# Optimization experiments

Hardware: AMD Instinct MI355X
Metric: run time of the kernel (lower is better)

The kernel has to match this reference:

```python
import jax, jax.numpy as jnp
import numpy as np

B, C_IN, HW = 4096, 3, 32
NUM_MODULES, NUM_AGENTS, OUT_DIM = 16, 10, 10
FEAT = 128
HID = 48
BN_EPS = 1e-5


def _conv_block(x, w, b):
    # x: [B,C,H,W], w: [O,I,3,3] -> conv(pad=1) + ReLU + maxpool2
    y = jax.lax.conv_general_dilated(
        x, w, window_strides=(1, 1), padding=((1, 1), (1, 1)),
        dimension_numbers=("NCHW", "OIHW", "NCHW"))
    y = jax.nn.relu(y + b[None, :, None, None])
    return jax.lax.reduce_window(y, -jnp.inf, jax.lax.max,
                                 (1, 1, 2, 2), (1, 1, 2, 2), "VALID")


def setup_inputs() -> dict:
    key = jax.random.key(0)
    ks = jax.random.split(key, 24)

    def lin(k, shape, fan_in):
        return (jax.random.normal(k, shape, dtype=jnp.float32) / np.sqrt(fan_in)).astype(jnp.float32)

    inp = {
        "x": jax.random.normal(ks[0], (B, C_IN, HW, HW), dtype=jnp.float32),
        "tasks": jax.random.randint(ks[1], (B,), 0, NUM_AGENTS, dtype=jnp.int32),
        # conv backbone
        "cw1": lin(ks[2], (32, C_IN, 3, 3), C_IN * 9), "cb1": jnp.zeros((32,), jnp.float32),
        "cw2": lin(ks[3], (32, 32, 3, 3), 32 * 9),     "cb2": jnp.zeros((32,), jnp.float32),
        "cw3": lin(ks[4], (32, 32, 3, 3), 32 * 9),     "cb3": jnp.zeros((32,), jnp.float32),
        "cw4": lin(ks[5], (32, 32, 3, 3), 32 * 9),     "cb4": jnp.zeros((32,), jnp.float32),
        "bn_g": jnp.ones((32,), jnp.float32), "bn_b": jnp.zeros((32,), jnp.float32),
        # routing policies (approx linear policies)
        "wpt": lin(ks[6], (FEAT, NUM_AGENTS), FEAT),                  # per-task assignment (1 agent)
        "wd1": lin(ks[7], (NUM_AGENTS, FEAT, NUM_MODULES), FEAT),    # per-agent decision 1
        "wd2": lin(ks[8], (NUM_AGENTS, HID, NUM_MODULES), HID),      # per-agent decision 2
        "wd3": lin(ks[9], (NUM_AGENTS, HID, NUM_MODULES), HID),      # per-agent decision 3
        # expert banks (stacked Linear layers, stored [in,out])
        "s1_w": lin(ks[10], (NUM_MODULES, FEAT, HID), FEAT), "s1_b": jnp.zeros((NUM_MODULES, HID), jnp.float32),
        "s2_w": lin(ks[11], (NUM_MODULES, HID, HID), HID),   "s2_b": jnp.zeros((NUM_MODULES, HID), jnp.float32),
        "s3_w": lin(ks[12], (NUM_MODULES, HID, OUT_DIM), HID), "s3_b": jnp.zeros((NUM_MODULES, OUT_DIM), jnp.float32),
    }
    return inp


def _decide(feat, wd, agents):
    # gather per-sample agent policy, pick argmax action
    logits = jnp.einsum("bf,bfm->bm", feat, wd[agents])  # [B, num_modules]
    return jnp.argmax(logits, axis=-1)


def _select(feat, w_bank, b_bank, actions, relu=True):
    # per-sample expert gather -> small GEMM -> scatter back (vectorized)
    y = jnp.einsum("bf,bfo->bo", feat, w_bank[actions]) + b_bank[actions]
    return jax.nn.relu(y) if relu else y


def reference(x, tasks, cw1, cb1, cw2, cb2, cw3, cb3, cw4, cb4, bn_g, bn_b,
              wpt, wd1, wd2, wd3, s1_w, s1_b, s2_w, s2_b, s3_w, s3_b):
    y = _conv_block(x, cw1, cb1)
    y = _conv_block(y, cw2, cb2)
    y = _conv_block(y, cw3, cb3)
    y = _conv_block(y, cw4, cb4)
    # BatchNorm2d (training-mode batch stats)
    mu = jnp.mean(y, axis=(0, 2, 3), keepdims=True)
    var = jnp.var(y, axis=(0, 2, 3), keepdims=True)
    y = (y - mu) * jax.lax.rsqrt(var + BN_EPS) * bn_g[None, :, None, None] + bn_b[None, :, None, None]
    y = y.reshape(y.shape[0], -1)  # [B, 128]

    # per-task assignment: single-agent policy picks the agent id per sample
    task_actions = jnp.argmax(y @ wpt, axis=-1)  # [B]

    a1 = _decide(y, wd1, task_actions)
    y = _select(y, s1_w, s1_b, a1, relu=True)
    a2 = _decide(y, wd2, task_actions)
    y = _select(y, s2_w, s2_b, a2, relu=True)
    a3 = _decide(y, wd3, task_actions)
    y = _select(y, s3_w, s3_b, a3, relu=False)
    return y
```

## Files before the change

### kernel.cpp

```cpp
#include <hip/hip_runtime.h>
#include <math.h>


#define IMG_B 4096

typedef _Float16 f16x8 __attribute__((ext_vector_type(8)));
typedef _Float16 f16x4 __attribute__((ext_vector_type(4)));
typedef float    f32x4 __attribute__((ext_vector_type(4)));

union U16x8 { unsigned u[4]; f16x8 v; };

__device__ inline f16x8 f16x8_zero() {
    f16x8 z;
    #pragma unroll
    for (int i = 0; i < 8; ++i) z[i] = (_Float16)0.f;
    return z;
}

__global__ __launch_bounds__(256) void twt_kernel(
    const float* __restrict__ cw1, const float* __restrict__ cw2,
    const float* __restrict__ cw3, const float* __restrict__ cw4,
    _Float16* __restrict__ w1s, _Float16* __restrict__ w2s,
    _Float16* __restrict__ w3s, _Float16* __restrict__ w4s)
{
    const int i = blockIdx.x * 256 + threadIdx.x;
    if (i < 2048) {
        const int p = i >> 10, rr = i & 1023;
        const int oc = rr >> 5, k = rr & 31;
        _Float16 val = (_Float16)0.f;
        if (k < 27) {
            float w = cw1[oc * 27 + k];
            _Float16 h = (_Float16)w;
            val = p ? (_Float16)(w - (float)h) : h;
        }
        w1s[p * 1024 + oc * 32 + k] = val;
    }
    if (i < 9216) {
        const int k = i % 9, r = i / 9;
        const int ic2 = r & 31, oc2 = r >> 5;
        {
            float w = cw2[(oc2 * 32 + ic2) * 9 + k];
            _Float16 h = (_Float16)w;
            w2s[(k * 2 + 0) * 1024 + oc2 * 32 + ic2] = h;
            w2s[(k * 2 + 1) * 1024 + oc2 * 32 + ic2] = (_Float16)(w - (float)h);
        }
        {
            float w = cw3[(oc2 * 32 + ic2) * 9 + k];
            _Float16 h = (_Float16)w;
            w3s[(k * 2 + 0) * 1024 + oc2 * 32 + ic2] = h;
            w3s[(k * 2 + 1) * 1024 + oc2 * 32 + ic2] = (_Float16)(w - (float)h);
        }
        {
            float w = cw4[(oc2 * 32 + ic2) * 9 + k];
            _Float16 h = (_Float16)w;
            w4s[(k * 2 + 0) * 1024 + oc2 * 32 + ic2] = h;
            w4s[(k * 2 + 1) * 1024 + oc2 * 32 + ic2] = (_Float16)(w - (float)h);
        }
    }
}

__global__ __launch_bounds__(512, 6) void backbone_kernel(
    const float* __restrict__ x,
    const _Float16* __restrict__ w1s, const float* __restrict__ cb1,
    const _Float16* __restrict__ w2s, const float* __restrict__ cb2,
    const _Float16* __restrict__ w3s, const float* __restrict__ cb3,
    const _Float16* __restrict__ w4s, const float* __restrict__ cb4,
    float* __restrict__ t4)
{
    __shared__ __align__(16) unsigned char smem[50736];
    _Float16* b1h = (_Float16*)smem;
    _Float16* b1l = (_Float16*)(smem + 18432);
    unsigned char* region2 = smem + 36864;
    unsigned* sxu = (unsigned*)region2;
    _Float16* b2h = (_Float16*)region2;
    _Float16* b2l = (_Float16*)(region2 + 4096);
    _Float16* b3h = (_Float16*)(region2 + 8192);
    _Float16* b3l = (_Float16*)(region2 + 10496);
    float*    scr = (float*)region2;

    const int t = threadIdx.x;
    const int b = blockIdx.x;
    const int lane = t & 63;
    const int w  = __builtin_amdgcn_readfirstlane(t >> 6);
    const int wr = w >> 1;
    const int mh = w & 1;
    const int xl = lane & 15;
    const int g  = lane >> 4;
    const int aoff = xl * 32 + g * 8;

    for (int i = t; i < 396; i += 512) {
        const int p = i / 132, r = i - p * 132;
        int row, col;
        if (r < 34)       { row = 0;       col = r; }
        else if (r < 68)  { row = 33;      col = r - 34; }
        else if (r < 100) { row = r - 67;  col = 0; }
        else              { row = r - 99;  col = 33; }
        sxu[p * 1156 + row * 34 + col] = 0;
    }
    for (int i = t; i < 1024; i += 512) {
        const int j = i & 15, cs = (i >> 4) & 1, r = (i >> 5) & 15, P = i >> 9;
        ((unsigned*)(smem + P * 18432))[(r * 18 + (cs ? 17 : 0)) * 16 + j] = 0;
    }
    {
        const float* xb = x + (size_t)b * 3072;
        for (int i = t; i < 3072; i += 512) {
            const int ic = i >> 10, r = i & 1023;
            const float v = xb[i];
            const _Float16 h = (_Float16)v;
            const _Float16 l = (_Float16)(v - (float)h);
            const unsigned hu = (unsigned)__builtin_bit_cast(unsigned short, h);
            const unsigned lu = (unsigned)__builtin_bit_cast(unsigned short, l);
            sxu[ic * 1156 + ((r >> 5) + 1) * 34 + (r & 31) + 1] =
                __builtin_amdgcn_perm(lu, hu, 0x05040100u);
        }
    }
    __syncthreads();

    {
        const f16x8 ah0 = *(const f16x8*)(w1s + xl * 32 + g * 8);
        const f16x8 ah1 = *(const f16x8*)(w1s + (16 + xl) * 32 + g * 8);
        const f16x8 al0 = *(const f16x8*)(w1s + 1024 + xl * 32 + g * 8);
        const f16x8 al1 = *(const f16x8*)(w1s + 1024 + (16 + xl) * 32 + g * 8);
        const f32x4 cbias0 = *(const f32x4*)(cb1 + g * 4);
        const f32x4 cbias1 = *(const f32x4*)(cb1 + 16 + g * 4);

        int off_j[8];
        #pragma unroll
        for (int j = 0; j < 8; ++j) {
            int k = g * 8 + j; if (k > 26) k = 26;
            const int ic = k / 9, t9 = k - ic * 9;
            const int dy = t9 / 3, dx = t9 - dy * 3;
            off_j[j] = ic * 1156 + dy * 34 + dx;
        }

        #pragma unroll
        for (int q = 0; q < 2; ++q) {
            const int rp = w * 2 + q;
            const int y0 = 2 * rp;
            #pragma unroll
            for (int xt = 0; xt < 2; ++xt) {
                const int xpix = xt * 16 + xl;
                f32x4 acc[2][2];
                #pragma unroll
                for (int yy = 0; yy < 2; ++yy)
                    #pragma unroll
                    for (int m = 0; m < 2; ++m)
                        #pragma unroll
                        for (int r = 0; r < 4; ++r) acc[yy][m][r] = 0.f;
                #pragma unroll
                for (int yy = 0; yy < 2; ++yy) {
                    const int base = (y0 + yy) * 34 + xpix;
                    unsigned e[8];
                    #pragma unroll
                    for (int j = 0; j < 8; ++j) e[j] = sxu[off_j[j] + base];
                    U16x8 Bh, Bl;
                    #pragma unroll
                    for (int p = 0; p < 4; ++p) {
                        const unsigned e0 = e[2 * p], e1 = e[2 * p + 1];
                        Bh.u[p] = __builtin_amdgcn_perm(e1, e0, 0x05040100u);
                        Bl.u[p] = __builtin_amdgcn_perm(e1, e0, 0x07060302u);
                    }
                    acc[yy][0] = __builtin_amdgcn_mfma_f32_16x16x32_f16(ah0, Bh.v, acc[yy][0], 0, 0, 0);
                    acc[yy][0] = __builtin_amdgcn_mfma_f32_16x16x32_f16(ah0, Bl.v, acc[yy][0], 0, 0, 0);
                    acc[yy][0] = __builtin_amdgcn_mfma_f32_16x16x32_f16(al0, Bh.v, acc[yy][0], 0, 0, 0);
                    acc[yy][1] = __builtin_amdgcn_mfma_f32_16x16x32_f16(ah1, Bh.v, acc[yy][1], 0, 0, 0);
                    acc[yy][1] = __builtin_amdgcn_mfma_f32_16x16x32_f16(ah1, Bl.v, acc[yy][1], 0, 0, 0);
                    acc[yy][1] = __builtin_amdgcn_mfma_f32_16x16x32_f16(al1, Bh.v, acc[yy][1], 0, 0, 0);
                }
                #pragma unroll
                for (int m = 0; m < 2; ++m) {
                    f32x4 vv;
                    #pragma unroll
                    for (int r = 0; r < 4; ++r) {
                        float v = fmaxf(acc[0][m][r], acc[1][m][r]);
                        v = fmaxf(v, __shfl_xor(v, 1));
                        vv[r] = fmaxf(v + (m ? cbias1[r] : cbias0[r]), 0.f);
                    }
                    if ((xl & 1) == 0) {
                        const int c = xt * 8 + (xl >> 1) + 1;
                        const int grp = m * 2 + (g >> 1);
                        const int so = (grp + (c >> 1)) & 3;
                        const int e = (rp * 18 + c) * 32 + so * 8 + (g & 1) * 4;
                        f16x4 h4, l4;
                        #pragma unroll
                        for (int r = 0; r < 4; ++r) {
                            const _Float16 h = (_Float16)vv[r];
                            h4[r] = h;
                            l4[r] = (_Float16)(vv[r] - (float)h);
                        }
                        *(f16x4*)(b1h + e) = h4;
                        *(f16x4*)(b1l + e) = l4;
                    }
                }
            }
        }
    }
    __syncthreads();

    {
        for (int i = t; i < 1152; i += 512) ((unsigned*)(region2 + 8192))[i] = 0;

        f32x4 acc[2][2];
        #pragma unroll
        for (int j = 0; j < 2; ++j)
            #pragma unroll
            for (int m = 0; m < 2; ++m)
                #pragma unroll
                for (int r = 0; r < 4; ++r) acc[j][m][r] = 0.f;

        #pragma unroll
        for (int dy = 0; dy < 3; ++dy) {
            #pragma unroll
            for (int dx = 0; dx < 3; ++dx) {
                const _Float16* wb = w2s + (dy * 3 + dx) * 2048;
                const f16x8 ah0 = *(const f16x8*)(wb + aoff);
                const f16x8 ah1 = *(const f16x8*)(wb + 512 + aoff);
                const f16x8 al0 = *(const f16x8*)(wb + 1024 + aoff);
                const f16x8 al1 = *(const f16x8*)(wb + 1536 + aoff);

                const int cxs = xl + dx;
                const int so = (g + (cxs >> 1)) & 3;
                #pragma unroll
                for (int j = 0; j < 2; ++j) {
                    const int sy = 2 * w + j + dy - 1;
                    if ((unsigned)sy < 16u) {
                        const int e = (sy * 18 + cxs) * 32 + so * 8;
                        const f16x8 bh = *(const f16x8*)(b1h + e);
                        const f16x8 bl = *(const f16x8*)(b1l + e);
                        acc[j][0] = __builtin_amdgcn_mfma_f32_16x16x32_f16(ah0, bh, acc[j][0], 0, 0, 0);
                        acc[j][0] = __builtin_amdgcn_mfma_f32_16x16x32_f16(ah0, bl, acc[j][0], 0, 0, 0);
                        acc[j][0] = __builtin_amdgcn_mfma_f32_16x16x32_f16(al0, bh, acc[j][0], 0, 0, 0);
                        acc[j][1] = __builtin_amdgcn_mfma_f32_16x16x32_f16(ah1, bh, acc[j][1], 0, 0, 0);
                        acc[j][1] = __builtin_amdgcn_mfma_f32_16x16x32_f16(ah1, bl, acc[j][1], 0, 0, 0);
                        acc[j][1] = __builtin_amdgcn_mfma_f32_16x16x32_f16(al1, bh, acc[j][1], 0, 0, 0);
                    }
                }
            }
        }

        const f32x4 bias0 = *(const f32x4*)(cb2 + g * 4);
        const f32x4 bias1 = *(const f32x4*)(cb2 + 16 + g * 4);
        #pragma unroll
        for (int m = 0; m < 2; ++m) {
            f32x4 vv;
            #pragma unroll
            for (int r = 0; r < 4; ++r) {
                float v = fmaxf(acc[0][m][r], acc[1][m][r]);
                v = fmaxf(v, __shfl_xor(v, 1));
                vv[r] = fmaxf(v + (m ? bias1[r] : bias0[r]), 0.f);
            }
            if ((lane & 1) == 0) {
                const int pp = w * 8 + (xl >> 1);
                const int slot = m * 2 + (g >> 1);
                const int so2 = (slot + (pp >> 1)) & 3;
                const int e = pp * 32 + so2 * 8 + (g & 1) * 4;
                f16x4 h4, l4;
                #pragma unroll
                for (int r = 0; r < 4; ++r) {
                    const _Float16 h = (_Float16)vv[r];
                    h4[r] = h;
                    l4[r] = (_Float16)(vv[r] - (float)h);
                }
                *(f16x4*)(b2h + e) = h4;
                *(f16x4*)(b2l + e) = l4;
            }
        }
    }
    __syncthreads();

    {
        const int p = wr * 16 + xl;
        const int py3 = p >> 3, px3 = p & 7;
        f32x4 acc;
        #pragma unroll
        for (int r = 0; r < 4; ++r) acc[r] = 0.f;

        #pragma unroll
        for (int dy = 0; dy < 3; ++dy) {
            #pragma unroll
            for (int dx = 0; dx < 3; ++dx) {
                const _Float16* wb = w3s + (dy * 3 + dx) * 2048 + mh * 512;
                const f16x8 ah = *(const f16x8*)(wb + aoff);
                const f16x8 al = *(const f16x8*)(wb + 1024 + aoff);

                const int syL = py3 + dy - 1, sxL = px3 + dx - 1;
                const bool ok = ((unsigned)syL < 8u) && ((unsigned)sxL < 8u);
                const int cy = syL < 0 ? 0 : (syL > 7 ? 7 : syL);
                const int cx = sxL < 0 ? 0 : (sxL > 7 ? 7 : sxL);
                const int cp = cy * 8 + cx;
                const int so = (g + (cp >> 1)) & 3;
                const int e = cp * 32 + so * 8;
                f16x8 bh = *(const f16x8*)(b2h + e);
                f16x8 bl = *(const f16x8*)(b2l + e);
                if (!ok) { bh = f16x8_zero(); bl = f16x8_zero(); }
                acc = __builtin_amdgcn_mfma_f32_16x16x32_f16(ah, bh, acc, 0, 0, 0);
                acc = __builtin_amdgcn_mfma_f32_16x16x32_f16(ah, bl, acc, 0, 0, 0);
                acc = __builtin_amdgcn_mfma_f32_16x16x32_f16(al, bh, acc, 0, 0, 0);
            }
        }

        const f32x4 bias = *(const f32x4*)(cb3 + mh * 16 + g * 4);
        f32x4 vv;
        #pragma unroll
        for (int r = 0; r < 4; ++r) {
            float v = acc[r];
            v = fmaxf(v, __shfl_xor(v, 1));
            v = fmaxf(v, __shfl_xor(v, 8));
            vv[r] = fmaxf(v + bias[r], 0.f);
        }
        if ((lane & 9) == 0) {
            const int yr = wr;
            const int xr = (xl & 7) >> 1;
            const int pp3 = (yr + 1) * 6 + (xr + 1);
            const int grp = mh * 2 + (g >> 1);
            const int so = (grp + (pp3 >> 1)) & 3;
            const int e = pp3 * 32 + so * 8 + (g & 1) * 4;
            f16x4 h4, l4;
            #pragma unroll
            for (int r = 0; r < 4; ++r) {
                const _Float16 h = (_Float16)vv[r];
                h4[r] = h;
                l4[r] = (_Float16)(vv[r] - (float)h);
            }
            *(f16x4*)(b3h + e) = h4;
            *(f16x4*)(b3l + e) = l4;
        }
    }
    __syncthreads();

    {
        f32x4 a4;
        #pragma unroll
        for (int r = 0; r < 4; ++r) a4[r] = 0.f;

        for (int t9 = wr; t9 < 9; t9 += 4) {
            const _Float16* wb = w4s + t9 * 2048 + mh * 512;
            const f16x8 ah = *(const f16x8*)(wb + aoff);
            const f16x8 al = *(const f16x8*)(wb + 1024 + aoff);
            const int dy = t9 / 3, dx = t9 - dy * 3;
            const int pp3 = ((xl >> 2) + dy) * 6 + (xl & 3) + dx;
            const int so = (g + (pp3 >> 1)) & 3;
            const int e = pp3 * 32 + so * 8;
            const f16x8 bh = *(const f16x8*)(b3h + e);
            const f16x8 bl = *(const f16x8*)(b3l + e);
            a4 = __builtin_amdgcn_mfma_f32_16x16x32_f16(ah, bh, a4, 0, 0, 0);
            a4 = __builtin_amdgcn_mfma_f32_16x16x32_f16(ah, bl, a4, 0, 0, 0);
            a4 = __builtin_amdgcn_mfma_f32_16x16x32_f16(al, bh, a4, 0, 0, 0);
        }
        *(f32x4*)(scr + (w * 64 + lane) * 4) = a4;
        __syncthreads();

        if (w < 2) {
            f32x4 r0;
            #pragma unroll
            for (int r = 0; r < 4; ++r) r0[r] = 0.f;
            #pragma unroll
            for (int k = 0; k < 4; ++k) {
                const f32x4 p0 = *(const f32x4*)(scr + ((k * 2 + w) * 64 + lane) * 4);
                #pragma unroll
                for (int r = 0; r < 4; ++r) r0[r] += p0[r];
            }
            const f32x4 bias = *(const f32x4*)(cb4 + w * 16 + g * 4);
            const int y = xl >> 2, xx = xl & 3;
            f32x4 vv;
            #pragma unroll
            for (int r = 0; r < 4; ++r) {
                float v = r0[r];
                v = fmaxf(v, __shfl_xor(v, 1));
                v = fmaxf(v, __shfl_xor(v, 4));
                vv[r] = fmaxf(v + bias[r], 0.f);
            }
            if ((xl & 5) == 0) {
                const int oc0 = w * 16 + g * 4;
                #pragma unroll
                for (int r = 0; r < 4; ++r)
                    t4[(size_t)b * 128 + (oc0 + r) * 4 + (y >> 1) * 2 + (xx >> 1)] = vv[r];
            }
        }
    }
}

__global__ __launch_bounds__(256) void bnstatsA_kernel(
    const float* __restrict__ t4, double* __restrict__ part)
{
    __shared__ double ssum[256];
    __shared__ double ssq[256];
    const int c = blockIdx.x >> 3, s = blockIdx.x & 7, t = threadIdx.x;
    const float* base = t4 + (size_t)s * 512 * 128 + c * 4;
    double sm = 0.0, q = 0.0;
    for (int j = t; j < 2048; j += 256) {
        const float v = base[(size_t)(j >> 2) * 128 + (j & 3)];
        sm += (double)v;
        q += (double)v * (double)v;
    }
    ssum[t] = sm; ssq[t] = q;
    __syncthreads();
    for (int w = 128; w > 0; w >>= 1) {
        if (t < w) { ssum[t] += ssum[t + w]; ssq[t] += ssq[t + w]; }
        __syncthreads();
    }
    if (t == 0) {
        part[(c * 8 + s) * 2]     = ssum[0];
        part[(c * 8 + s) * 2 + 1] = ssq[0];
    }
}

__global__ __launch_bounds__(256) void bnstatsB_kernel(
    const double* __restrict__ part, float* __restrict__ mus, float* __restrict__ rss)
{
    const int t = threadIdx.x;
    double sm = part[t * 2], q = part[t * 2 + 1];
    #pragma unroll
    for (int d = 1; d < 8; d <<= 1) {
        sm += __shfl_xor(sm, d);
        q += __shfl_xor(q, d);
    }
    if ((t & 7) == 0) {
        const double mu = sm / 16384.0;
        const double var = q / 16384.0 - mu * mu;
        mus[t >> 3] = (float)mu;
        rss[t >> 3] = (float)(1.0 / sqrt(var + 1e-5));
    }
}

__device__ __forceinline__ int wave_argmax16(double v, int idx) {
    #pragma unroll
    for (int d = 8; d >= 1; d >>= 1) {
        const double ov = __shfl_xor(v, d);
        const int oi = __shfl_xor(idx, d);
        if (ov > v || (ov == v && oi < idx)) { v = ov; idx = oi; }
    }
    return __shfl(idx, 0);
}

__global__ __launch_bounds__(256) void routing_kernel(
    const float* __restrict__ t4, const float* __restrict__ mus,
    const float* __restrict__ rss,
    const float* __restrict__ bng, const float* __restrict__ bnb,
    const float* __restrict__ wpt, const float* __restrict__ wd1,
    const float* __restrict__ wd2, const float* __restrict__ wd3,
    const float* __restrict__ s1w, const float* __restrict__ s1b,
    const float* __restrict__ s2w, const float* __restrict__ s2b,
    const float* __restrict__ s3w, const float* __restrict__ s3b,
    float* __restrict__ out)
{
    __shared__ float fs[4][128];
    __shared__ float h1s[4][48];
    __shared__ float h2s[4][48];
    const int t = threadIdx.x & 63;
    const int w = threadIdx.x >> 6;
    const int b = blockIdx.x * 4 + w;
    float* fw  = fs[w];
    float* h1w = h1s[w];
    float* h2w = h2s[w];

    for (int i = t; i < 128; i += 64) {
        const int c = i >> 2;
        const float v = t4[(size_t)b * 128 + i];
        fw[i] = (v - mus[c]) * rss[c] * bng[c] + bnb[c];
    }
    __builtin_amdgcn_wave_barrier();

    double a = -INFINITY;
    if (t < 10) {
        double s0 = 0, s1 = 0, s2 = 0, s3 = 0;
        for (int k = 0; k < 128; k += 4) {
            s0 = fma((double)fw[k],     (double)wpt[k * 10 + t],       s0);
            s1 = fma((double)fw[k + 1], (double)wpt[(k + 1) * 10 + t], s1);
            s2 = fma((double)fw[k + 2], (double)wpt[(k + 2) * 10 + t], s2);
            s3 = fma((double)fw[k + 3], (double)wpt[(k + 3) * 10 + t], s3);
        }
        a = (s0 + s1) + (s2 + s3);
    }
    const int agent = wave_argmax16(a, t & 15);

    a = -INFINITY;
    if (t < 16) {
        const float* wd = wd1 + (size_t)agent * 2048 + t;
        double s0 = 0, s1 = 0, s2 = 0, s3 = 0;
        for (int k = 0; k < 128; k += 4) {
            s0 = fma((double)fw[k],     (double)wd[k * 16],       s0);
            s1 = fma((double)fw[k + 1], (double)wd[(k + 1) * 16], s1);
            s2 = fma((double)fw[k + 2], (double)wd[(k + 2) * 16], s2);
            s3 = fma((double)fw[k + 3], (double)wd[(k + 3) * 16], s3);
        }
        a = (s0 + s1) + (s2 + s3);
    }
    const int a1 = wave_argmax16(a, t & 15);

    if (t < 48) {
        const float* wd = s1w + (size_t)a1 * 6144 + t;
        float c0 = s1b[a1 * 48 + t], c1 = 0.f, c2 = 0.f, c3 = 0.f;
        for (int k = 0; k < 128; k += 4) {
            c0 = fmaf(fw[k],     wd[k * 48],       c0);
            c1 = fmaf(fw[k + 1], wd[(k + 1) * 48], c1);
            c2 = fmaf(fw[k + 2], wd[(k + 2) * 48], c2);
            c3 = fmaf(fw[k + 3], wd[(k + 3) * 48], c3);
        }
        h1w[t] = fmaxf((c0 + c1) + (c2 + c3), 0.f);
    }
    __builtin_amdgcn_wave_barrier();

    a = -INFINITY;
    if (t < 16) {
        const float* wd = wd2 + (size_t)agent * 768 + t;
        double s0 = 0, s1 = 0, s2 = 0, s3 = 0;
        for (int k = 0; k < 48; k += 4) {
            s0 = fma((double)h1w[k],     (double)wd[k * 16],       s0);
            s1 = fma((double)h1w[k + 1], (double)wd[(k + 1) * 16], s1);
            s2 = fma((double)h1w[k + 2], (double)wd[(k + 2) * 16], s2);
            s3 = fma((double)h1w[k + 3], (double)wd[(k + 3) * 16], s3);
        }
        a = (s0 + s1) + (s2 + s3);
    }
    const int a2 = wave_argmax16(a, t & 15);

    if (t < 48) {
        const float* wd = s2w + (size_t)a2 * 2304 + t;
        float c0 = s2b[a2 * 48 + t], c1 = 0.f, c2 = 0.f, c3 = 0.f;
        for (int k = 0; k < 48; k += 4) {
            c0 = fmaf(h1w[k],     wd[k * 48],       c0);
            c1 = fmaf(h1w[k + 1], wd[(k + 1) * 48], c1);
            c2 = fmaf(h1w[k + 2], wd[(k + 2) * 48], c2);
            c3 = fmaf(h1w[k + 3], wd[(k + 3) * 48], c3);
        }
        h2w[t] = fmaxf((c0 + c1) + (c2 + c3), 0.f);
    }
    __builtin_amdgcn_wave_barrier();

    a = -INFINITY;
    if (t < 16) {
        const float* wd = wd3 + (size_t)agent * 768 + t;
        double s0 = 0, s1 = 0, s2 = 0, s3 = 0;
        for (int k = 0; k < 48; k += 4) {
            s0 = fma((double)h2w[k],     (double)wd[k * 16],       s0);
            s1 = fma((double)h2w[k + 1], (double)wd[(k + 1) * 16], s1);
            s2 = fma((double)h2w[k + 2], (double)wd[(k + 2) * 16], s2);
            s3 = fma((double)h2w[k + 3], (double)wd[(k + 3) * 16], s3);
        }
        a = (s0 + s1) + (s2 + s3);
    }
    const int a3 = wave_argmax16(a, t & 15);

    if (t < 10) {
        const float* wd = s3w + (size_t)a3 * 480 + t;
        float c0 = s3b[a3 * 10 + t], c1 = 0.f, c2 = 0.f, c3 = 0.f;
        for (int k = 0; k < 48; k += 4) {
            c0 = fmaf(h2w[k],     wd[k * 10],       c0);
            c1 = fmaf(h2w[k + 1], wd[(k + 1) * 10], c1);
            c2 = fmaf(h2w[k + 2], wd[(k + 2) * 10], c2);
            c3 = fmaf(h2w[k + 3], wd[(k + 3) * 10], c3);
        }
        out[(size_t)b * 10 + t] = (c0 + c1) + (c2 + c3);
    }
}

extern "C" void kernel_launch(void* const* d_in, const int* in_sizes, int n_in,
                              void* d_out, int out_size, void* d_ws, size_t ws_size,
                              hipStream_t stream)
{
    (void)in_sizes; (void)n_in; (void)out_size; (void)ws_size;

    const float* x   = (const float*)d_in[0];
    const float* cw1 = (const float*)d_in[2];
    const float* cb1 = (const float*)d_in[3];
    const float* cw2 = (const float*)d_in[4];
    const float* cb2 = (const float*)d_in[5];
    const float* cw3 = (const float*)d_in[6];
    const float* cb3 = (const float*)d_in[7];
    const float* cw4 = (const float*)d_in[8];
    const float* cb4 = (const float*)d_in[9];
    const float* bng = (const float*)d_in[10];
    const float* bnb = (const float*)d_in[11];
    const float* wpt = (const float*)d_in[12];
    const float* wd1 = (const float*)d_in[13];
    const float* wd2 = (const float*)d_in[14];
    const float* wd3 = (const float*)d_in[15];
    const float* s1w = (const float*)d_in[16];
    const float* s1b = (const float*)d_in[17];
    const float* s2w = (const float*)d_in[18];
    const float* s2b = (const float*)d_in[19];
    const float* s3w = (const float*)d_in[20];
    const float* s3b = (const float*)d_in[21];
    float* out = (float*)d_out;

    float* t4  = (float*)d_ws;
    float* mus = t4 + (size_t)IMG_B * 128;
    float* rss = mus + 32;
    _Float16* w1s = (_Float16*)(rss + 32);
    _Float16* w2s = w1s + 2048;
    _Float16* w3s = w2s + 18432;
    _Float16* w4s = w3s + 18432;
    double* part = (double*)(w4s + 18432);

    hipLaunchKernelGGL(twt_kernel, dim3(36), dim3(256), 0, stream,
                       cw1, cw2, cw3, cw4, w1s, w2s, w3s, w4s);
    hipLaunchKernelGGL(backbone_kernel, dim3(IMG_B), dim3(512), 0, stream,
                       x, w1s, cb1, w2s, cb2, w3s, cb3, w4s, cb4, t4);
    hipLaunchKernelGGL(bnstatsA_kernel, dim3(256), dim3(256), 0, stream, t4, part);
    hipLaunchKernelGGL(bnstatsB_kernel, dim3(1), dim3(256), 0, stream, part, mus, rss);
    hipLaunchKernelGGL(routing_kernel, dim3(IMG_B / 4), dim3(256), 0, stream,
                       t4, mus, rss, bng, bnb, wpt, wd1, wd2, wd3,
                       s1w, s1b, s2w, s2b, s3w, s3b, out);
}
```

Measured before the change: 175.2 us.

## Spill layer-1 low-half activation buffer to global memory to raise occupancy

Adds a templated backbone variant that keeps the low-order fp16 half of the layer-1 output in a per-block global workspace instead of LDS. LDS use per block drops from about 50 KB to 32 KB, and the launch-bounds min-blocks hint rises from 6 to 8 to allow more resident blocks. The variant is chosen at run time when the workspace is large enough. The cost is global/L2 traffic (about 75 MB of writes and reads across the batch) and higher latency on every access to that buffer.

```diff
diff --git a/kernel.cpp b/kernel.cpp
--- a/kernel.cpp
+++ b/kernel.cpp
@@ -59,18 +59,20 @@
     }
 }
 
-__global__ __launch_bounds__(512, 6) void backbone_kernel(
+template<bool SPILL>
+__global__ __launch_bounds__(512, SPILL ? 8 : 6) void backbone_kernel(
     const float* __restrict__ x,
     const _Float16* __restrict__ w1s, const float* __restrict__ cb1,
     const _Float16* __restrict__ w2s, const float* __restrict__ cb2,
     const _Float16* __restrict__ w3s, const float* __restrict__ cb3,
     const _Float16* __restrict__ w4s, const float* __restrict__ cb4,
-    float* __restrict__ t4)
+    _Float16* __restrict__ b1lg, float* __restrict__ t4)
 {
-    __shared__ __align__(16) unsigned char smem[50736];
+    constexpr int SMEM_BYTES = SPILL ? 32304 : 50736;
+    constexpr int R2_OFF     = SPILL ? 18432 : 36864;
+    __shared__ __align__(16) unsigned char smem[SMEM_BYTES];
     _Float16* b1h = (_Float16*)smem;
-    _Float16* b1l = (_Float16*)(smem + 18432);
-    unsigned char* region2 = smem + 36864;
+    unsigned char* region2 = smem + R2_OFF;
     unsigned* sxu = (unsigned*)region2;
     _Float16* b2h = (_Float16*)region2;
     _Float16* b2l = (_Float16*)(region2 + 4096);
@@ -80,6 +82,11 @@
 
     const int t = threadIdx.x;
     const int b = blockIdx.x;
+
+    _Float16* b1l;
+    if constexpr (SPILL) b1l = b1lg + (size_t)b * 9216;
+    else                 b1l = (_Float16*)(smem + 18432);
+
     const int lane = t & 63;
     const int w  = __builtin_amdgcn_readfirstlane(t >> 6);
     const int wr = w >> 1;
@@ -97,9 +104,18 @@
         else              { row = r - 99;  col = 33; }
         sxu[p * 1156 + row * 34 + col] = 0;
     }
-    for (int i = t; i < 1024; i += 512) {
-        const int j = i & 15, cs = (i >> 4) & 1, r = (i >> 5) & 15, P = i >> 9;
-        ((unsigned*)(smem + P * 18432))[(r * 18 + (cs ? 17 : 0)) * 16 + j] = 0;
+    if constexpr (SPILL) {
+        if (t < 512) {
+            const int j = t & 15, cs = (t >> 4) & 1, r = (t >> 5) & 15;
+            const int e = (r * 18 + (cs ? 17 : 0)) * 16 + j;
+            ((unsigned*)b1h)[e] = 0;
+            ((unsigned*)b1l)[e] = 0;
+        }
+    } else {
+        for (int i = t; i < 1024; i += 512) {
+            const int j = i & 15, cs = (i >> 4) & 1, r = (i >> 5) & 15, P = i >> 9;
+            ((unsigned*)(smem + P * 18432))[(r * 18 + (cs ? 17 : 0)) * 16 + j] = 0;
+        }
     }
     {
         const float* xb = x + (size_t)b * 3072;
@@ -559,7 +575,7 @@
                               void* d_out, int out_size, void* d_ws, size_t ws_size,
                               hipStream_t stream)
 {
-    (void)in_sizes; (void)n_in; (void)out_size; (void)ws_size;
+    (void)in_sizes; (void)n_in; (void)out_size;
 
     const float* x   = (const float*)d_in[0];
     const float* cw1 = (const float*)d_in[2];
@@ -592,11 +608,20 @@
     _Float16* w3s = w2s + 18432;
     _Float16* w4s = w3s + 18432;
     double* part = (double*)(w4s + 18432);
+    _Float16* b1lg = (_Float16*)(part + 512);
+
+    const size_t need = (size_t)((char*)(b1lg + (size_t)IMG_B * 9216) - (char*)d_ws);
+    const bool spill = (ws_size >= need);
 
     hipLaunchKernelGGL(twt_kernel, dim3(36), dim3(256), 0, stream,
                        cw1, cw2, cw3, cw4, w1s, w2s, w3s, w4s);
-    hipLaunchKernelGGL(backbone_kernel, dim3(IMG_B), dim3(512), 0, stream,
-                       x, w1s, cb1, w2s, cb2, w3s, cb3, w4s, cb4, t4);
+    if (spill) {
+        hipLaunchKernelGGL((backbone_kernel<true>), dim3(IMG_B), dim3(512), 0, stream,
+                           x, w1s, cb1, w2s, cb2, w3s, cb3, w4s, cb4, b1lg, t4);
+    } else {
+        hipLaunchKernelGGL((backbone_kernel<false>), dim3(IMG_B), dim3(512), 0, stream,
+                           x, w1s, cb1, w2s, cb2, w3s, cb3, w4s, cb4, b1lg, t4);
+    }
     hipLaunchKernelGGL(bnstatsA_kernel, dim3(256), dim3(256), 0, stream, t4, part);
     hipLaunchKernelGGL(bnstatsB_kernel, dim3(1), dim3(256), 0, stream, part, mus, rss);
     hipLaunchKernelGGL(routing_kernel, dim3(IMG_B / 4), dim3(256), 0, stream,
```

New measurement: 258.2 us. 1.47x slower.
